# Performance work log

Hardware: AMD Instinct MI355X
Metric: run time of the kernel (lower is better)

The kernel has to match this reference:

```python
import jax, jax.numpy as jnp
import numpy as np
from jax import lax

N, C, H, W = 32, 256, 56, 56
SHIFT = 2  # p_5_1_0, frozen random.randint(-3,3)

def setup_inputs() -> dict:
    key = jax.random.key(0)
    k1, k2, k3 = jax.random.split(key, 3)
    x = jax.random.normal(k1, (N, C, H, W), dtype=jnp.float32)
    w6 = jax.random.normal(k2, (C, 1), dtype=jnp.float32) * 0.1  # trunc_normal(std=0.1) approx
    w7 = jax.random.normal(k3, (C, C * 25), dtype=jnp.float32) * (1.0 / np.sqrt(C * 25))
    return {"x": x, "w6": w6, "w7": w7}

def reference(x, w6, w7):
    # t_1: max over width -> (n,c,h)
    t1 = jnp.max(x, axis=3)
    # t_3/t_4: relu then tanh
    t4 = jnp.tanh(jax.nn.relu(x))
    # t_5: roll along height axis
    t5 = jnp.roll(x, SHIFT, axis=2)
    # t_6: einsum 'abcd,be->aecd' with e=1 -> (n,h,w)
    t6 = jnp.einsum('nchw,c->nhw', t4, w6[:, 0])
    # t_2 + p_7: unfold(5x5, dilation=3, padding=6) + 1x1 conv == dilated 5x5 conv.
    # unfold channel ordering is c*25 + (kh*5+kw), so reshape to OIHW directly.
    conv_w = w7.reshape(C, C, 5, 5)
    t7 = lax.conv_general_dilated(
        x, conv_w, window_strides=(1, 1), padding=[(6, 6), (6, 6)],
        rhs_dilation=(3, 3), dimension_numbers=('NCHW', 'OIHW', 'NCHW'))
    t8 = x * t7
    # t_9: softmax over width of (n,h,w)
    t9 = jax.nn.softmax(t6, axis=2)
    t10 = t9[:, None, :, :] * t5
    t11 = t10 + t8
    return t1[:, :, :, None] - t11
```

## Files before the change

kernel.cpp:

```cpp
#include <hip/hip_runtime.h>
#include <hip/hip_bf16.h>
#include <math.h>

typedef __bf16 bf16x8 __attribute__((ext_vector_type(8)));
typedef short  s16x8  __attribute__((ext_vector_type(8)));
typedef float  f32x16 __attribute__((ext_vector_type(16)));
typedef unsigned short u16;

#define NN 32
#define CC 256
#define HH 56
#define WW 56
#define HP 68
#define XP2_BYTES 75759616ull
#define XP2_OFF 0ull
#define WT3_OFF 75759616ull
#define T1_OFF  79036416ull
#define T9_OFF  80871424ull

__device__ inline u16 f2bf(float f) {
    unsigned int u = __builtin_bit_cast(unsigned int, f);
    u = (u + 0x7fffu + ((u >> 16) & 1u)) >> 16;
    return (u16)u;
}

__device__ inline void gl_lds16(const char* g, char* l) {
    __builtin_amdgcn_global_load_lds(
        (const __attribute__((address_space(1))) unsigned int*)g,
        (__attribute__((address_space(3))) unsigned int*)l, 16, 0, 0);
}

__global__ void zero_halo(u16* __restrict__ xp2) {
    const int total = NN * 1488 * 32;
    int i = blockIdx.x * blockDim.x + threadIdx.x;
    const int stride = gridDim.x * blockDim.x;
    uint4 z; z.x = z.y = z.z = z.w = 0u;
    for (; i < total; i += stride) {
        int chunk = i & 31;
        int pid = i >> 5;
        int n = pid / 1488;
        int hp = pid - n * 1488;
        int row, col;
        if (hp < 816) { int r = hp / 68; col = hp - r * 68; row = (r < 6) ? r : r + 56; }
        else { int hq = hp - 816; int rr = hq / 12; int c12 = hq - rr * 12;
               row = 6 + rr; col = (c12 < 6) ? c12 : c12 + 56; }
        *(uint4*)((char*)xp2 + ((((size_t)n * HP + row) * HP + col) * 512) + chunk * 16) = z;
    }
}

__global__ __launch_bounds__(256)
void pack_w(const float* __restrict__ w7, u16* __restrict__ wt3) {
    int idx = blockIdx.x * 256 + threadIdx.x;
    int c_out = idx / 6400;
    int k = idx - c_out * 6400;
    int cin = k / 25;
    int tap = k - cin * 25;
    int kn = tap * 8 + (cin >> 5);
    int c5 = cin & 31;
    int ks = c5 >> 4, half = (c5 >> 3) & 1, j = c5 & 7;
    int lane = half * 32 + (c_out & 31);
    int rb = c_out >> 5;
    wt3[(size_t)kn * 8192 + ks * 4096 + rb * 512 + lane * 8 + j] = f2bf(w7[idx]);
}

__global__ __launch_bounds__(256)
void t169(const float* __restrict__ x, const float* __restrict__ w6,
          float* __restrict__ t1, float* __restrict__ t9) {
    const int n = blockIdx.x / HH;
    const int h = blockIdx.x % HH;
    const int wave = threadIdx.x >> 6;
    const int lane = threadIdx.x & 63;
    const bool valid = lane < WW;
    const int wl = valid ? lane : (WW - 1);
    const float* xrow = x + ((size_t)(n * CC) * HH + h) * WW;
    float a0 = 0.f, a1 = 0.f, a2 = 0.f, a3 = 0.f;
    __shared__ float sbuf[4 * 64];
    for (int i0 = 0; i0 < 64; i0 += 4) {
        const int c = wave * 64 + i0;
        float x0 = xrow[(size_t)(c + 0) * (HH * WW) + wl];
        float x1 = xrow[(size_t)(c + 1) * (HH * WW) + wl];
        float x2 = xrow[(size_t)(c + 2) * (HH * WW) + wl];
        float x3 = xrow[(size_t)(c + 3) * (HH * WW) + wl];
        float m0 = valid ? x0 : -INFINITY;
        float m1 = valid ? x1 : -INFINITY;
        float m2 = valid ? x2 : -INFINITY;
        float m3 = valid ? x3 : -INFINITY;
#pragma unroll
        for (int off = 32; off > 0; off >>= 1) {
            m0 = fmaxf(m0, __shfl_xor(m0, off));
            m1 = fmaxf(m1, __shfl_xor(m1, off));
            m2 = fmaxf(m2, __shfl_xor(m2, off));
            m3 = fmaxf(m3, __shfl_xor(m3, off));
        }
        if (lane == 0) {
            t1[(size_t)(n * CC + c + 0) * HH + h] = m0;
            t1[(size_t)(n * CC + c + 1) * HH + h] = m1;
            t1[(size_t)(n * CC + c + 2) * HH + h] = m2;
            t1[(size_t)(n * CC + c + 3) * HH + h] = m3;
        }
        if (valid) {
            float e0 = __expf(2.f * fmaxf(x0, 0.f));
            float e1 = __expf(2.f * fmaxf(x1, 0.f));
            float e2 = __expf(2.f * fmaxf(x2, 0.f));
            float e3 = __expf(2.f * fmaxf(x3, 0.f));
            a0 += (1.f - 2.f * __builtin_amdgcn_rcpf(e0 + 1.f)) * w6[c + 0];
            a1 += (1.f - 2.f * __builtin_amdgcn_rcpf(e1 + 1.f)) * w6[c + 1];
            a2 += (1.f - 2.f * __builtin_amdgcn_rcpf(e2 + 1.f)) * w6[c + 2];
            a3 += (1.f - 2.f * __builtin_amdgcn_rcpf(e3 + 1.f)) * w6[c + 3];
        }
    }
    sbuf[wave * 64 + lane] = (a0 + a1) + (a2 + a3);
    __syncthreads();
    if (wave == 0) {
        float s = sbuf[lane] + sbuf[64 + lane] + sbuf[128 + lane] + sbuf[192 + lane];
        float sm = valid ? s : -INFINITY;
        float mx = sm;
#pragma unroll
        for (int off = 32; off > 0; off >>= 1)
            mx = fmaxf(mx, __shfl_xor(mx, off));
        float e = valid ? expf(s - mx) : 0.f;
        float tot = e;
#pragma unroll
        for (int off = 32; off > 0; off >>= 1)
            tot += __shfl_xor(tot, off);
        if (valid) t9[((size_t)n * HH + h) * WW + lane] = e / tot;
    }
}

__global__ __launch_bounds__(256)
void pack_x(const float* __restrict__ x, u16* __restrict__ xp2) {
    const int n = blockIdx.x / HH;
    const int h = blockIdx.x % HH;
    const int lane = threadIdx.x & 63;
    const int wid = threadIdx.x >> 6;
    __shared__ u16 xbuf[64 * 66];
    const float* xrow = x + ((size_t)(n * CC) * HH + h) * WW;
    u16* dst = xp2 + (((size_t)n * HP + h + 6) * HP + 6) * CC;
    for (int g = 0; g < 4; ++g) {
        if (g) __syncthreads();
        if (lane < WW) {
            const int c0 = g * 64 + wid * 16;
#pragma unroll
            for (int r = 0; r < 16; ++r) {
                float v = xrow[(size_t)(c0 + r) * (HH * WW) + lane];
                xbuf[(wid * 16 + r) * 66 + lane] = f2bf(v);
            }
        }
        __syncthreads();
        for (int id = threadIdx.x; id < WW * 8; id += 256) {
            int p = id >> 3, ch8 = id & 7;
            s16x8 pk;
#pragma unroll
            for (int j = 0; j < 8; ++j)
                pk[j] = (short)xbuf[(ch8 * 8 + j) * 66 + p];
            *(s16x8*)(dst + (size_t)p * CC + g * 64 + ch8 * 8) = pk;
        }
    }
}

__global__ __launch_bounds__(512, 2)
void conv_main(const char* __restrict__ xp2b, const char* __restrict__ wt3b,
               const float* __restrict__ x, const float* __restrict__ t1,
               const float* __restrict__ t9, float* __restrict__ out) {
    extern __shared__ __align__(16) char smem[];
    const int bid = blockIdx.x;
    const int tile = (bid & 7) * 49 + (bid >> 3);
    const int tid  = threadIdx.x;
    const int wid  = tid >> 6;
    const int lane = tid & 63;
    const int l31 = lane & 31;
    const int lhi = lane >> 5;
    const int wr = wid >> 2;
    const int wc = wid & 3;

    unsigned vb;
    {
        int p = tile * 256 + wid * 32 + l31;
        int n = p / (HH * WW);
        int rem = p - n * (HH * WW);
        int hh = rem / WW;
        int ww = rem - hh * WW;
        vb = ((((unsigned)n * HP + hh + 6) * HP) + ww + 6) * 512 + lhi * 16;
    }

    auto stageA = [&](int tt, int ks) {
        const int kn = (tt < 200) ? tt : (tt - 200);
        const unsigned o = ks * 8192 + wid * 1024 + lane * 16;
        char* d = smem + (size_t)(tt & 3) * 32768 + o;
        const char* g = wt3b + (size_t)kn * 16384 + o;
        gl_lds16(g, d);
    };
    auto stageB = [&](int tt, int ks) {
        const int kn = (tt < 200) ? tt : (tt - 200);
        const int tp = kn >> 3, ch = kn & 7;
        const char* gb = xp2b +
            (ptrdiff_t)((tp / 5) * 3 - 6) * (HP * 512) +
            (ptrdiff_t)((tp % 5) * 3 - 6) * 512 + ch * 64 + ks * 32 + vb;
        char* d = smem + (size_t)(tt & 3) * 32768 + 16384
                  + ks * 8192 + wid * 1024 + lane * 16;
        gl_lds16(gb, d);
    };

    f32x16 acc[4][2];
#pragma unroll
    for (int mi = 0; mi < 4; ++mi)
#pragma unroll
        for (int nb = 0; nb < 2; ++nb)
#pragma unroll
            for (int r = 0; r < 16; ++r)
                acc[mi][nb][r] = 0.f;

    const int aoff = wr * 4096 + lane * 16;
    const int boff = 16384 + wc * 2048 + lane * 16;

#pragma unroll
    for (int tt = 0; tt < 3; ++tt) {
        stageA(tt, 0); stageB(tt, 0);
        stageA(tt, 1); stageB(tt, 1);
    }
    asm volatile("s_waitcnt vmcnt(8)" ::: "memory");
    __builtin_amdgcn_s_barrier();

    for (int t = 0; t < 200; ++t) {
        const char* bp = smem + (size_t)(t & 3) * 32768;
        bf16x8 av[4], bv[2];

#pragma unroll
        for (int ks = 0; ks < 2; ++ks) {
            stageA(t + 3, ks); stageB(t + 3, ks);
#pragma unroll
            for (int nb = 0; nb < 2; ++nb)
                bv[nb] = *(const bf16x8*)(const void*)(bp + boff + ks * 8192 + nb * 1024);
#pragma unroll
            for (int mi = 0; mi < 4; ++mi)
                av[mi] = *(const bf16x8*)(const void*)(bp + aoff + ks * 8192 + mi * 1024);
            __builtin_amdgcn_s_setprio(1);
#pragma unroll
            for (int mi = 0; mi < 4; ++mi)
#pragma unroll
                for (int nb = 0; nb < 2; ++nb)
                    acc[mi][nb] = __builtin_amdgcn_mfma_f32_32x32x16_bf16(
                        av[mi], bv[nb], acc[mi][nb], 0, 0, 0);
            __builtin_amdgcn_s_setprio(0);
        }
        asm volatile("s_waitcnt vmcnt(8)" ::: "memory");
        __builtin_amdgcn_s_barrier();
    }

#pragma unroll
    for (int nb = 0; nb < 2; ++nb) {
        const int p = tile * 256 + wc * 64 + nb * 32 + l31;
        const int n = p / (HH * WW);
        const int rem = p - n * (HH * WW);
        const int h = rem / WW;
        const int w = rem - h * WW;
        const float t9v = t9[((size_t)n * HH + h) * WW + w];
        const int hprev = (h >= 2) ? (h - 2) : (h + HH - 2);
#pragma unroll
        for (int mi = 0; mi < 4; ++mi) {
            const int c0 = wr * 128 + mi * 32 + 4 * lhi;
#pragma unroll
            for (int r = 0; r < 16; ++r) {
                const int c = c0 + (r & 3) + 8 * (r >> 2);
                const size_t rowi = (size_t)(n * CC + c) * HH;
                const float t1v = t1[rowi + h];
                const float xv = x[(rowi + h) * WW + w];
                const float xr = x[(rowi + hprev) * WW + w];
                out[(rowi + h) * WW + w] = t1v - (t9v * xr + xv * acc[mi][nb][r]);
            }
        }
    }
}

extern "C" void kernel_launch(void* const* d_in, const int* in_sizes, int n_in,
                              void* d_out, int out_size, void* d_ws, size_t ws_size,
                              hipStream_t stream) {
    const float* x  = (const float*)d_in[0];
    const float* w6 = (const float*)d_in[1];
    const float* w7 = (const float*)d_in[2];
    float* out = (float*)d_out;
    char* ws = (char*)d_ws;
    u16*   xp2 = (u16*)(ws + XP2_OFF);
    u16*   wt3 = (u16*)(ws + WT3_OFF);
    float* t1  = (float*)(ws + T1_OFF);
    float* t9  = (float*)(ws + T9_OFF);

    static bool lds_cfg_done = false;
    if (!lds_cfg_done) {
        (void)hipFuncSetAttribute((const void*)conv_main,
                                  hipFuncAttributeMaxDynamicSharedMemorySize,
                                  131072);
        lds_cfg_done = true;
    }

    zero_halo<<<dim3(1024), dim3(256), 0, stream>>>(xp2);
    pack_w<<<dim3(6400), dim3(256), 0, stream>>>(w7, wt3);
    t169<<<dim3(NN * HH), dim3(256), 0, stream>>>(x, w6, t1, t9);
    pack_x<<<dim3(NN * HH), dim3(256), 0, stream>>>(x, xp2);
    conv_main<<<dim3(392), dim3(512), 131072, stream>>>((const char*)xp2, (const char*)wt3,
                                                        x, t1, t9, out);
}
```

Measured before the change: 618.5 us.

## Fuse max/softmax prep with bf16 pack of x and unroll conv main loop by four

Merges the t1/t9 reduction kernel with the x bf16 transpose-pack kernel, so x is read from global memory once and one launch is dropped. Separately, the conv main loop is unrolled by four ring-buffer stages, with all stage loads for a step issued before its MFMAs, so buffer offsets become compile-time constants. The fused kernel serialises the reductions with the LDS transpose per channel group, and the larger unroll raises code size and register pressure.

```diff
diff --git a/kernel.cpp b/kernel.cpp
--- a/kernel.cpp
+++ b/kernel.cpp
@@ -64,54 +64,76 @@
 }
 
 __global__ __launch_bounds__(256)
-void t169(const float* __restrict__ x, const float* __restrict__ w6,
-          float* __restrict__ t1, float* __restrict__ t9) {
+void prep(const float* __restrict__ x, const float* __restrict__ w6,
+          float* __restrict__ t1, float* __restrict__ t9,
+          u16* __restrict__ xp2) {
     const int n = blockIdx.x / HH;
     const int h = blockIdx.x % HH;
-    const int wave = threadIdx.x >> 6;
     const int lane = threadIdx.x & 63;
+    const int wid = threadIdx.x >> 6;
     const bool valid = lane < WW;
     const int wl = valid ? lane : (WW - 1);
+    __shared__ u16 xbuf[64 * 66];
+    __shared__ float sbuf[4 * 64];
     const float* xrow = x + ((size_t)(n * CC) * HH + h) * WW;
-    float a0 = 0.f, a1 = 0.f, a2 = 0.f, a3 = 0.f;
-    __shared__ float sbuf[4 * 64];
-    for (int i0 = 0; i0 < 64; i0 += 4) {
-        const int c = wave * 64 + i0;
-        float x0 = xrow[(size_t)(c + 0) * (HH * WW) + wl];
-        float x1 = xrow[(size_t)(c + 1) * (HH * WW) + wl];
-        float x2 = xrow[(size_t)(c + 2) * (HH * WW) + wl];
-        float x3 = xrow[(size_t)(c + 3) * (HH * WW) + wl];
-        float m0 = valid ? x0 : -INFINITY;
-        float m1 = valid ? x1 : -INFINITY;
-        float m2 = valid ? x2 : -INFINITY;
-        float m3 = valid ? x3 : -INFINITY;
-#pragma unroll
-        for (int off = 32; off > 0; off >>= 1) {
-            m0 = fmaxf(m0, __shfl_xor(m0, off));
-            m1 = fmaxf(m1, __shfl_xor(m1, off));
-            m2 = fmaxf(m2, __shfl_xor(m2, off));
-            m3 = fmaxf(m3, __shfl_xor(m3, off));
-        }
-        if (lane == 0) {
-            t1[(size_t)(n * CC + c + 0) * HH + h] = m0;
-            t1[(size_t)(n * CC + c + 1) * HH + h] = m1;
-            t1[(size_t)(n * CC + c + 2) * HH + h] = m2;
-            t1[(size_t)(n * CC + c + 3) * HH + h] = m3;
-        }
-        if (valid) {
-            float e0 = __expf(2.f * fmaxf(x0, 0.f));
-            float e1 = __expf(2.f * fmaxf(x1, 0.f));
-            float e2 = __expf(2.f * fmaxf(x2, 0.f));
-            float e3 = __expf(2.f * fmaxf(x3, 0.f));
-            a0 += (1.f - 2.f * __builtin_amdgcn_rcpf(e0 + 1.f)) * w6[c + 0];
-            a1 += (1.f - 2.f * __builtin_amdgcn_rcpf(e1 + 1.f)) * w6[c + 1];
-            a2 += (1.f - 2.f * __builtin_amdgcn_rcpf(e2 + 1.f)) * w6[c + 2];
-            a3 += (1.f - 2.f * __builtin_amdgcn_rcpf(e3 + 1.f)) * w6[c + 3];
-        }
-    }
-    sbuf[wave * 64 + lane] = (a0 + a1) + (a2 + a3);
+    u16* dst = xp2 + (((size_t)n * HP + h + 6) * HP + 6) * CC;
+    float accw = 0.f;
+    for (int g = 0; g < 4; ++g) {
+        if (g) __syncthreads();
+        const int c0 = g * 64 + wid * 16;
+#pragma unroll
+        for (int r0 = 0; r0 < 16; r0 += 4) {
+            float xv0 = xrow[(size_t)(c0 + r0 + 0) * (HH * WW) + wl];
+            float xv1 = xrow[(size_t)(c0 + r0 + 1) * (HH * WW) + wl];
+            float xv2 = xrow[(size_t)(c0 + r0 + 2) * (HH * WW) + wl];
+            float xv3 = xrow[(size_t)(c0 + r0 + 3) * (HH * WW) + wl];
+            if (valid) {
+                xbuf[(wid * 16 + r0 + 0) * 66 + lane] = f2bf(xv0);
+                xbuf[(wid * 16 + r0 + 1) * 66 + lane] = f2bf(xv1);
+                xbuf[(wid * 16 + r0 + 2) * 66 + lane] = f2bf(xv2);
+                xbuf[(wid * 16 + r0 + 3) * 66 + lane] = f2bf(xv3);
+            }
+            float m0 = valid ? xv0 : -INFINITY;
+            float m1 = valid ? xv1 : -INFINITY;
+            float m2 = valid ? xv2 : -INFINITY;
+            float m3 = valid ? xv3 : -INFINITY;
+#pragma unroll
+            for (int off = 32; off > 0; off >>= 1) {
+                m0 = fmaxf(m0, __shfl_xor(m0, off));
+                m1 = fmaxf(m1, __shfl_xor(m1, off));
+                m2 = fmaxf(m2, __shfl_xor(m2, off));
+                m3 = fmaxf(m3, __shfl_xor(m3, off));
+            }
+            if (lane == 0) {
+                t1[(size_t)(n * CC + c0 + r0 + 0) * HH + h] = m0;
+                t1[(size_t)(n * CC + c0 + r0 + 1) * HH + h] = m1;
+                t1[(size_t)(n * CC + c0 + r0 + 2) * HH + h] = m2;
+                t1[(size_t)(n * CC + c0 + r0 + 3) * HH + h] = m3;
+            }
+            if (valid) {
+                float e0 = __expf(2.f * fmaxf(xv0, 0.f));
+                float e1 = __expf(2.f * fmaxf(xv1, 0.f));
+                float e2 = __expf(2.f * fmaxf(xv2, 0.f));
+                float e3 = __expf(2.f * fmaxf(xv3, 0.f));
+                accw += (1.f - 2.f * __builtin_amdgcn_rcpf(e0 + 1.f)) * w6[c0 + r0 + 0];
+                accw += (1.f - 2.f * __builtin_amdgcn_rcpf(e1 + 1.f)) * w6[c0 + r0 + 1];
+                accw += (1.f - 2.f * __builtin_amdgcn_rcpf(e2 + 1.f)) * w6[c0 + r0 + 2];
+                accw += (1.f - 2.f * __builtin_amdgcn_rcpf(e3 + 1.f)) * w6[c0 + r0 + 3];
+            }
+        }
+        __syncthreads();
+        for (int id = threadIdx.x; id < WW * 8; id += 256) {
+            int p = id >> 3, ch8 = id & 7;
+            s16x8 pk;
+#pragma unroll
+            for (int j = 0; j < 8; ++j)
+                pk[j] = (short)xbuf[(ch8 * 8 + j) * 66 + p];
+            *(s16x8*)(dst + (size_t)p * CC + g * 64 + ch8 * 8) = pk;
+        }
+    }
+    sbuf[wid * 64 + lane] = accw;
     __syncthreads();
-    if (wave == 0) {
+    if (wid == 0) {
         float s = sbuf[lane] + sbuf[64 + lane] + sbuf[128 + lane] + sbuf[192 + lane];
         float sm = valid ? s : -INFINITY;
         float mx = sm;
@@ -124,37 +146,6 @@
         for (int off = 32; off > 0; off >>= 1)
             tot += __shfl_xor(tot, off);
         if (valid) t9[((size_t)n * HH + h) * WW + lane] = e / tot;
-    }
-}
-
-__global__ __launch_bounds__(256)
-void pack_x(const float* __restrict__ x, u16* __restrict__ xp2) {
-    const int n = blockIdx.x / HH;
-    const int h = blockIdx.x % HH;
-    const int lane = threadIdx.x & 63;
-    const int wid = threadIdx.x >> 6;
-    __shared__ u16 xbuf[64 * 66];
-    const float* xrow = x + ((size_t)(n * CC) * HH + h) * WW;
-    u16* dst = xp2 + (((size_t)n * HP + h + 6) * HP + 6) * CC;
-    for (int g = 0; g < 4; ++g) {
-        if (g) __syncthreads();
-        if (lane < WW) {
-            const int c0 = g * 64 + wid * 16;
-#pragma unroll
-            for (int r = 0; r < 16; ++r) {
-                float v = xrow[(size_t)(c0 + r) * (HH * WW) + lane];
-                xbuf[(wid * 16 + r) * 66 + lane] = f2bf(v);
-            }
-        }
-        __syncthreads();
-        for (int id = threadIdx.x; id < WW * 8; id += 256) {
-            int p = id >> 3, ch8 = id & 7;
-            s16x8 pk;
-#pragma unroll
-            for (int j = 0; j < 8; ++j)
-                pk[j] = (short)xbuf[(ch8 * 8 + j) * 66 + p];
-            *(s16x8*)(dst + (size_t)p * CC + g * 64 + ch8 * 8) = pk;
-        }
     }
 }
 
@@ -221,30 +212,34 @@
     asm volatile("s_waitcnt vmcnt(8)" ::: "memory");
     __builtin_amdgcn_s_barrier();
 
-    for (int t = 0; t < 200; ++t) {
-        const char* bp = smem + (size_t)(t & 3) * 32768;
-        bf16x8 av[4], bv[2];
-
-#pragma unroll
-        for (int ks = 0; ks < 2; ++ks) {
-            stageA(t + 3, ks); stageB(t + 3, ks);
-#pragma unroll
-            for (int nb = 0; nb < 2; ++nb)
-                bv[nb] = *(const bf16x8*)(const void*)(bp + boff + ks * 8192 + nb * 1024);
-#pragma unroll
-            for (int mi = 0; mi < 4; ++mi)
-                av[mi] = *(const bf16x8*)(const void*)(bp + aoff + ks * 8192 + mi * 1024);
-            __builtin_amdgcn_s_setprio(1);
-#pragma unroll
-            for (int mi = 0; mi < 4; ++mi)
+    for (int tb = 0; tb < 200; tb += 4) {
+#pragma unroll
+        for (int u = 0; u < 4; ++u) {
+            const int t = tb + u;
+            const char* bp = smem + (size_t)u * 32768;
+            stageA(t + 3, 0); stageB(t + 3, 0);
+            stageA(t + 3, 1); stageB(t + 3, 1);
+            bf16x8 av[4], bv[2];
+#pragma unroll
+            for (int ks = 0; ks < 2; ++ks) {
 #pragma unroll
                 for (int nb = 0; nb < 2; ++nb)
-                    acc[mi][nb] = __builtin_amdgcn_mfma_f32_32x32x16_bf16(
-                        av[mi], bv[nb], acc[mi][nb], 0, 0, 0);
-            __builtin_amdgcn_s_setprio(0);
-        }
-        asm volatile("s_waitcnt vmcnt(8)" ::: "memory");
-        __builtin_amdgcn_s_barrier();
+                    bv[nb] = *(const bf16x8*)(const void*)(bp + boff + ks * 8192 + nb * 1024);
+#pragma unroll
+                for (int mi = 0; mi < 4; ++mi)
+                    av[mi] = *(const bf16x8*)(const void*)(bp + aoff + ks * 8192 + mi * 1024);
+                __builtin_amdgcn_s_setprio(1);
+#pragma unroll
+                for (int mi = 0; mi < 4; ++mi)
+#pragma unroll
+                    for (int nb = 0; nb < 2; ++nb)
+                        acc[mi][nb] = __builtin_amdgcn_mfma_f32_32x32x16_bf16(
+                            av[mi], bv[nb], acc[mi][nb], 0, 0, 0);
+                __builtin_amdgcn_s_setprio(0);
+            }
+            asm volatile("s_waitcnt vmcnt(8)" ::: "memory");
+            __builtin_amdgcn_s_barrier();
+        }
     }
 
 #pragma unroll
@@ -295,8 +290,7 @@
 
     zero_halo<<<dim3(1024), dim3(256), 0, stream>>>(xp2);
     pack_w<<<dim3(6400), dim3(256), 0, stream>>>(w7, wt3);
-    t169<<<dim3(NN * HH), dim3(256), 0, stream>>>(x, w6, t1, t9);
-    pack_x<<<dim3(NN * HH), dim3(256), 0, stream>>>(x, xp2);
+    prep<<<dim3(NN * HH), dim3(256), 0, stream>>>(x, w6, t1, t9, xp2);
     conv_main<<<dim3(392), dim3(512), 131072, stream>>>((const char*)xp2, (const char*)wt3,
                                                         x, t1, t9, out);
 }
```

Result: no change. 629.8 us (+1.8%).
